# Kernel tuning notes

Hardware: AMD Instinct MI355X
Metric: run time of the kernel (lower is better)

Reference implementation:

```python
import jax, jax.numpy as jnp
import numpy as np

# Module hyperparameters (from init_kwargs)
LATENT = 1024
H = 16          # num query heads
HK = 4          # num key/value heads (GQA)
D = 64          # head_dim
CAUSAL = True
QKV_OUT = (3 * H + 2 * HK) * D  # 3584, as defined in the source module


def setup_inputs() -> dict:
    key = jax.random.key(0)
    k1, k2, k3 = jax.random.split(key, 3)
    B, S = 2, 2048
    x = jax.random.normal(k1, (B, S, LATENT), dtype=jnp.float32)
    # nn.Linear weights are [out_features, in_features]; scale like torch default init
    w_qkv = jax.random.normal(k2, (QKV_OUT, LATENT), dtype=jnp.float32) / np.sqrt(LATENT)
    w_out = jax.random.normal(k3, (LATENT, H * D), dtype=jnp.float32) / np.sqrt(H * D)
    return {"x": x, "w_qkv": w_qkv, "w_out": w_out}


def reference(x, w_qkv, w_out):
    B, S, _ = x.shape
    scale = 1.0 / np.sqrt(D).astype(np.float32)

    # Fused QKV projection: [B,S,(3H+2HK)*D]
    qkv = jnp.einsum('bsl,ol->bso', x, w_qkv)

    # Split: q takes H heads, k and v take HK heads each (GQA).
    # (The extra 2*H*D columns of the fused projection are allocated by the
    #  source module but unused by q/k/v, matching its layer sizing.)
    q = qkv[..., : H * D].reshape(B, S, H, D)
    k = qkv[..., H * D:(H + HK) * D].reshape(B, S, HK, D)
    v = qkv[..., (H + HK) * D:(H + 2 * HK) * D].reshape(B, S, HK, D)

    # Expand KV heads to match query heads (group factor H // HK)
    rep = H // HK
    k = jnp.repeat(k, rep, axis=2)  # [B,S,H,D]
    v = jnp.repeat(v, rep, axis=2)

    # Scaled dot-product attention
    scores = jnp.einsum('bshd,bthd->bhst', q, k) * scale  # [B,H,S,S]
    if CAUSAL:
        causal_mask = jnp.tril(jnp.ones((S, S), dtype=bool))
        scores = jnp.where(causal_mask, scores, jnp.finfo(scores.dtype).min)
    attn = jax.nn.softmax(scores, axis=-1)
    out = jnp.einsum('bhst,bthd->bshd', attn, v).reshape(B, S, H * D)

    # Output projection back to latent_size
    return jnp.einsum('bso,lo->bsl', out, w_out)
```

## Files before the change

kernel.cpp:

```cpp
#include <hip/hip_runtime.h>
#include <hip/hip_bf16.h>
#include <math.h>

typedef __attribute__((ext_vector_type(8))) short bf16x8;
typedef __attribute__((ext_vector_type(4))) float f32x4;
typedef unsigned short u16;
typedef unsigned int   u32;

#define DEVINL __device__ __forceinline__

DEVINL u16 f2bf(float x) {
    u32 u = __float_as_uint(x);
    u += 0x7fffu + ((u >> 16) & 1u);
    return (u16)(u >> 16);
}

DEVINL void gl_lds16(const void* g, void* s) {
    __builtin_amdgcn_global_load_lds(
        (const __attribute__((address_space(1))) u32*)g,
        (__attribute__((address_space(3))) u32*)s,
        16, 0, 0);
}

DEVINL f32x4 mfma16(bf16x8 a, bf16x8 b, f32x4 c) {
    return __builtin_amdgcn_mfma_f32_16x16x32_bf16(a, b, c, 0, 0, 0);
}

__global__ void cvt3(const float* __restrict__ x, const float* __restrict__ wq,
                     const float* __restrict__ wo,
                     u16* __restrict__ xb, u16* __restrict__ wqb, u16* __restrict__ wob) {
    int i = blockIdx.x * 256 + threadIdx.x;
    const float* s; u16* d; int j;
    if (i < 1048576)      { s = x;  d = xb;  j = i; }
    else if (i < 1441792) { s = wq; d = wqb; j = i - 1048576; }
    else                  { s = wo; d = wob; j = i - 1441792; }
    float4 v = ((const float4*)s)[j];
    ushort4 o;
    o.x = f2bf(v.x); o.y = f2bf(v.y); o.z = f2bf(v.z); o.w = f2bf(v.w);
    ((ushort4*)d)[j] = o;
}

template<int EP>
__launch_bounds__(128)
__global__ void gemm_w2(const u16* __restrict__ A, const u16* __restrict__ B,
                        const int N, const int K,
                        float* __restrict__ Cf,
                        u16* __restrict__ Qo, u16* __restrict__ Ko, u16* __restrict__ Vo)
{
    __shared__ __align__(16) u16 As[64 * 64];
    __shared__ __align__(16) u16 Bs[128 * 64];
    const int tid  = threadIdx.x;
    const int lane = tid & 63;
    const int quad = lane >> 4;
    const int lcol = lane & 15;
    const int w    = tid >> 6;
    const int lr   = lane >> 3;
    const int lc   = lane & 7;
    const int swst = lc ^ lr;
    const int rk   = lcol & 7;
    const int m0 = blockIdx.y * 64;
    const int n0 = blockIdx.x * 128;

    f32x4 acc[4][4];
    for (int mb = 0; mb < 4; mb++)
        for (int nb = 0; nb < 4; nb++)
            for (int i = 0; i < 4; i++) acc[mb][nb][i] = 0.f;

    const u16* Ap = A + (m0 + w * 32 + lr) * K + swst * 8;
    const u16* Bp = B + (n0 + w * 64 + lr) * K + swst * 8;

    for (int k0 = 0; k0 < K; k0 += 64) {
        for (int j = 0; j < 4; j++)
            gl_lds16(Ap + j * 8 * K + k0, As + (w * 32 + j * 8) * 64);
        for (int j = 0; j < 8; j++)
            gl_lds16(Bp + j * 8 * K + k0, Bs + (w * 64 + j * 8) * 64);
        __syncthreads();
        bf16x8 af[4][2], bfv[4][2];
        for (int ks = 0; ks < 2; ks++) {
            const int ch = ((ks * 4 + quad) ^ rk) * 8;
            for (int mb = 0; mb < 4; mb++)
                af[mb][ks] = *(const bf16x8*)&As[(mb * 16 + lcol) * 64 + ch];
            for (int nb = 0; nb < 4; nb++)
                bfv[nb][ks] = *(const bf16x8*)&Bs[(w * 64 + nb * 16 + lcol) * 64 + ch];
        }
        for (int ks = 0; ks < 2; ks++)
            for (int mb = 0; mb < 4; mb++)
                for (int nb = 0; nb < 4; nb++)
                    acc[mb][nb] = mfma16(af[mb][ks], bfv[nb][ks], acc[mb][nb]);
        __syncthreads();
    }

    if (EP == 0) {
        for (int mb = 0; mb < 4; mb++)
            for (int nb = 0; nb < 4; nb++) {
                int row = m0 + mb * 16 + quad * 4;
                int col = n0 + w * 64 + nb * 16 + lcol;
                for (int i = 0; i < 4; i++)
                    Cf[(row + i) * N + col] = acc[mb][nb][i];
            }
    } else {
        const float qsc = 0.18033688011112042f;
        for (int mb = 0; mb < 4; mb++)
            for (int nb = 0; nb < 4; nb++)
                for (int i = 0; i < 4; i++) {
                    int row = m0 + mb * 16 + quad * 4 + i;
                    int col = n0 + w * 64 + nb * 16 + lcol;
                    int bb = row >> 11, ss = row & 2047;
                    if (col < 1024) {
                        int hh = col >> 6, dd = col & 63;
                        Qo[((bb * 16 + hh) * 2048 + ss) * 64 + dd] = f2bf(acc[mb][nb][i] * qsc);
                    } else if (col < 1280) {
                        int c = col - 1024, hh = c >> 6, dd = c & 63;
                        Ko[((bb * 4 + hh) * 2048 + ss) * 64 + dd] = f2bf(acc[mb][nb][i]);
                    } else {
                        int c = col - 1280, hh = c >> 6, dd = c & 63;
                        Vo[((bb * 4 + hh) * 64 + dd) * 2048 + ss] = f2bf(acc[mb][nb][i]);
                    }
                }
    }
}

__launch_bounds__(128)
__global__ void attn_kernel(const u16* __restrict__ Qg, const u16* __restrict__ Kg,
                            const u16* __restrict__ Vtg, u16* __restrict__ Og)
{
    __shared__ __align__(16) u16 Ks[2][64 * 64];
    __shared__ __align__(16) u16 Vs[2][64 * 64];
    __shared__ __align__(16) u16 Ps[32 * 64];

    const int tid  = threadIdx.x;
    const int lane = tid & 63;
    const int w    = tid >> 6;
    const int quad = lane >> 4;
    const int lcol = lane & 15;
    const int lr   = lane >> 3;
    const int lc   = lane & 7;
    const int swst = lc ^ lr;
    const int rk   = lcol & 7;

    const int p  = blockIdx.x;
    const int h  = blockIdx.y;
    const int b  = blockIdx.z;
    const int hk = h >> 2;

    const u16* Qp = Qg  + (b * 16 + h) * 2048 * 64;
    const u16* Kp = Kg  + (b * 4 + hk) * 2048 * 64;
    const u16* Vp = Vtg + (b * 4 + hk) * 64 * 2048;

    for (int pass = 0; pass < 2; pass++) {
        const int qi = pass ? (63 - p) : p;
        const int q0 = qi * 32;
        const int nt = (qi >> 1) + 1;

        bf16x8 aqr[2];
        for (int ks = 0; ks < 2; ks++)
            aqr[ks] = *(const bf16x8*)(Qp + (q0 + w * 16 + lcol) * 64 + ks * 32 + quad * 8);

        for (int j = 0; j < 4; j++) {
            const int r = w * 32 + j * 8 + lr;
            gl_lds16(Kp + r * 64 + swst * 8,   &Ks[0][(w * 32 + j * 8) * 64]);
            gl_lds16(Vp + r * 2048 + swst * 8, &Vs[0][(w * 32 + j * 8) * 64]);
        }

        f32x4 o[4];
        float l_p[4];
        for (int db = 0; db < 4; db++)
            for (int i = 0; i < 4; i++) o[db][i] = 0.f;
        for (int i = 0; i < 4; i++) l_p[i] = 0.f;

        __syncthreads();

        for (int ti = 0; ti < nt; ti++) {
            const int cur = ti & 1;
            if (ti + 1 < nt) {
                const int nb = cur ^ 1;
                const int t0n = (ti + 1) * 64;
                for (int j = 0; j < 4; j++) {
                    const int r = w * 32 + j * 8 + lr;
                    gl_lds16(Kp + (t0n + r) * 64 + swst * 8, &Ks[nb][(w * 32 + j * 8) * 64]);
                    gl_lds16(Vp + r * 2048 + t0n + swst * 8, &Vs[nb][(w * 32 + j * 8) * 64]);
                }
            }

            f32x4 s[4];
            for (int cb = 0; cb < 4; cb++)
                for (int i = 0; i < 4; i++) s[cb][i] = 0.f;
            for (int ks = 0; ks < 2; ks++) {
                const int chq = ((ks * 4 + quad) ^ rk) * 8;
                for (int cb = 0; cb < 4; cb++) {
                    bf16x8 bk = *(const bf16x8*)&Ks[cur][(cb * 16 + lcol) * 64 + chq];
                    s[cb] = mfma16(aqr[ks], bk, s[cb]);
                }
            }

            if (ti == nt - 1) {
                const int t0 = ti * 64;
                for (int cb = 0; cb < 4; cb++)
                    for (int i = 0; i < 4; i++) {
                        const int rg = q0 + w * 16 + quad * 4 + i;
                        const int cg = t0 + cb * 16 + lcol;
                        s[cb][i] = (cg > rg) ? -INFINITY : s[cb][i];
                    }
            }

            for (int cb = 0; cb < 4; cb++)
                for (int i = 0; i < 4; i++) {
                    const float pv = exp2f(s[cb][i]);
                    s[cb][i] = pv;
                    l_p[i] += pv;
                }

            for (int cb = 0; cb < 4; cb++)
                for (int i = 0; i < 4; i++) {
                    const int rl = quad * 4 + i;
                    const int cc = cb * 2 + (lcol >> 3);
                    Ps[(w * 16 + rl) * 64 + ((cc ^ (rl & 7)) << 3) + lc] =
                        (u16)(__float_as_uint(s[cb][i]) >> 16);
                }

            for (int kt = 0; kt < 2; kt++) {
                const int chp = ((kt * 4 + quad) ^ rk) * 8;
                bf16x8 ap = *(const bf16x8*)&Ps[(w * 16 + lcol) * 64 + chp];
                for (int db = 0; db < 4; db++) {
                    bf16x8 bv = *(const bf16x8*)&Vs[cur][(db * 16 + lcol) * 64 + chp];
                    o[db] = mfma16(ap, bv, o[db]);
                }
            }
            __syncthreads();
        }

        for (int i = 0; i < 4; i++) {
            float l = l_p[i];
            for (int x = 1; x < 16; x <<= 1) l += __shfl_xor(l, x);
            const float inv = 1.0f / l;
            const int srow = q0 + w * 16 + quad * 4 + i;
            for (int db = 0; db < 4; db++)
                Og[(b * 2048 + srow) * 1024 + h * 64 + db * 16 + lcol] = f2bf(o[db][i] * inv);
        }
    }
}

extern "C" void kernel_launch(void* const* d_in, const int* in_sizes, int n_in,
                              void* d_out, int out_size, void* d_ws, size_t ws_size,
                              hipStream_t stream) {
    const float* x     = (const float*)d_in[0];
    const float* w_qkv = (const float*)d_in[1];
    const float* w_out = (const float*)d_in[2];
    float* out = (float*)d_out;
    char* ws = (char*)d_ws;

    u16* xb  = (u16*)(ws);
    u16* wqb = (u16*)(ws + 8  * 1024 * 1024);
    u16* wob = (u16*)(ws + 11 * 1024 * 1024);
    u16* qb  = (u16*)(ws + 13 * 1024 * 1024);
    u16* kb  = (u16*)(ws + 21 * 1024 * 1024);
    u16* vtb = (u16*)(ws + 23 * 1024 * 1024);
    u16* aob = (u16*)(ws);

    cvt3<<<6656, 256, 0, stream>>>(x, w_qkv, w_out, xb, wqb, wob);

    gemm_w2<1><<<dim3(12, 64), 128, 0, stream>>>(xb, wqb, 1536, 1024,
                                                 nullptr, qb, kb, vtb);
    attn_kernel<<<dim3(32, 16, 2), 128, 0, stream>>>(qb, kb, vtb, aob);
    gemm_w2<0><<<dim3(8, 64), 128, 0, stream>>>(aob, wob, 1024, 1024,
                                                out, nullptr, nullptr, nullptr);
}
```

Measured before the change: 180.9 us.

## Double GEMM K-step to 128 and use 64-row query tiles with 4 waves in attention

The projection GEMM now loads two 64-wide K slices per barrier pair, halving the number of synchronizations per K loop at the cost of doubled LDS. The attention kernel moves from 32-row to 64-row query tiles with 256 threads (4 waves), so each K/V tile loaded into LDS is shared by more query rows and grid size halves. The causal mask is simplified because query and key tiles now align at 64. Fewer blocks and larger LDS may reduce occupancy, and the part of the attention kernel not shown must match the new indexing.

```diff
diff --git a/kernel.cpp b/kernel.cpp
--- a/kernel.cpp
+++ b/kernel.cpp
@@ -47,8 +47,8 @@
                         float* __restrict__ Cf,
                         u16* __restrict__ Qo, u16* __restrict__ Ko, u16* __restrict__ Vo)
 {
-    __shared__ __align__(16) u16 As[64 * 64];
-    __shared__ __align__(16) u16 Bs[128 * 64];
+    __shared__ __align__(16) u16 As[2][64 * 64];
+    __shared__ __align__(16) u16 Bs[2][128 * 64];
     const int tid  = threadIdx.x;
     const int lane = tid & 63;
     const int quad = lane >> 4;
@@ -69,24 +69,27 @@
     const u16* Ap = A + (m0 + w * 32 + lr) * K + swst * 8;
     const u16* Bp = B + (n0 + w * 64 + lr) * K + swst * 8;
 
-    for (int k0 = 0; k0 < K; k0 += 64) {
-        for (int j = 0; j < 4; j++)
-            gl_lds16(Ap + j * 8 * K + k0, As + (w * 32 + j * 8) * 64);
-        for (int j = 0; j < 8; j++)
-            gl_lds16(Bp + j * 8 * K + k0, Bs + (w * 64 + j * 8) * 64);
+    for (int k0 = 0; k0 < K; k0 += 128) {
+        for (int h = 0; h < 2; h++)
+            for (int j = 0; j < 4; j++)
+                gl_lds16(Ap + j * 8 * K + h * 64 + k0, &As[h][(w * 32 + j * 8) * 64]);
+        for (int h = 0; h < 2; h++)
+            for (int j = 0; j < 8; j++)
+                gl_lds16(Bp + j * 8 * K + h * 64 + k0, &Bs[h][(w * 64 + j * 8) * 64]);
         __syncthreads();
-        bf16x8 af[4][2], bfv[4][2];
-        for (int ks = 0; ks < 2; ks++) {
-            const int ch = ((ks * 4 + quad) ^ rk) * 8;
+        for (int ks = 0; ks < 4; ks++) {
+            const int c  = ks * 4 + quad;
+            const int hh = c >> 3;
+            const int ch = ((c & 7) ^ rk) * 8;
+            bf16x8 af[4], bfv[4];
             for (int mb = 0; mb < 4; mb++)
-                af[mb][ks] = *(const bf16x8*)&As[(mb * 16 + lcol) * 64 + ch];
+                af[mb] = *(const bf16x8*)&As[hh][(mb * 16 + lcol) * 64 + ch];
             for (int nb = 0; nb < 4; nb++)
-                bfv[nb][ks] = *(const bf16x8*)&Bs[(w * 64 + nb * 16 + lcol) * 64 + ch];
-        }
-        for (int ks = 0; ks < 2; ks++)
+                bfv[nb] = *(const bf16x8*)&Bs[hh][(w * 64 + nb * 16 + lcol) * 64 + ch];
             for (int mb = 0; mb < 4; mb++)
                 for (int nb = 0; nb < 4; nb++)
-                    acc[mb][nb] = mfma16(af[mb][ks], bfv[nb][ks], acc[mb][nb]);
+                    acc[mb][nb] = mfma16(af[mb], bfv[nb], acc[mb][nb]);
+        }
         __syncthreads();
     }
 
@@ -120,13 +123,13 @@
     }
 }
 
-__launch_bounds__(128)
+__launch_bounds__(256)
 __global__ void attn_kernel(const u16* __restrict__ Qg, const u16* __restrict__ Kg,
                             const u16* __restrict__ Vtg, u16* __restrict__ Og)
 {
     __shared__ __align__(16) u16 Ks[2][64 * 64];
     __shared__ __align__(16) u16 Vs[2][64 * 64];
-    __shared__ __align__(16) u16 Ps[32 * 64];
+    __shared__ __align__(16) u16 Ps[64 * 64];
 
     const int tid  = threadIdx.x;
     const int lane = tid & 63;
@@ -148,18 +151,18 @@
     const u16* Vp = Vtg + (b * 4 + hk) * 64 * 2048;
 
     for (int pass = 0; pass < 2; pass++) {
-        const int qi = pass ? (63 - p) : p;
-        const int q0 = qi * 32;
-        const int nt = (qi >> 1) + 1;
+        const int qi = pass ? (31 - p) : p;
+        const int q0 = qi * 64;
+        const int nt = qi + 1;
 
         bf16x8 aqr[2];
         for (int ks = 0; ks < 2; ks++)
             aqr[ks] = *(const bf16x8*)(Qp + (q0 + w * 16 + lcol) * 64 + ks * 32 + quad * 8);
 
-        for (int j = 0; j < 4; j++) {
-            const int r = w * 32 + j * 8 + lr;
-            gl_lds16(Kp + r * 64 + swst * 8,   &Ks[0][(w * 32 + j * 8) * 64]);
-            gl_lds16(Vp + r * 2048 + swst * 8, &Vs[0][(w * 32 + j * 8) * 64]);
+        for (int j = 0; j < 2; j++) {
+            const int r = w * 16 + j * 8 + lr;
+            gl_lds16(Kp + r * 64 + swst * 8,   &Ks[0][w * 1024 + j * 512]);
+            gl_lds16(Vp + r * 2048 + swst * 8, &Vs[0][w * 1024 + j * 512]);
         }
 
         f32x4 o[4];
@@ -175,10 +178,10 @@
             if (ti + 1 < nt) {
                 const int nb = cur ^ 1;
                 const int t0n = (ti + 1) * 64;
-                for (int j = 0; j < 4; j++) {
-                    const int r = w * 32 + j * 8 + lr;
-                    gl_lds16(Kp + (t0n + r) * 64 + swst * 8, &Ks[nb][(w * 32 + j * 8) * 64]);
-                    gl_lds16(Vp + r * 2048 + t0n + swst * 8, &Vs[nb][(w * 32 + j * 8) * 64]);
+                for (int j = 0; j < 2; j++) {
+                    const int r = w * 16 + j * 8 + lr;
+                    gl_lds16(Kp + (t0n + r) * 64 + swst * 8, &Ks[nb][w * 1024 + j * 512]);
+                    gl_lds16(Vp + r * 2048 + t0n + swst * 8, &Vs[nb][w * 1024 + j * 512]);
                 }
             }
 
@@ -194,12 +197,10 @@
             }
 
             if (ti == nt - 1) {
-                const int t0 = ti * 64;
                 for (int cb = 0; cb < 4; cb++)
                     for (int i = 0; i < 4; i++) {
-                        const int rg = q0 + w * 16 + quad * 4 + i;
-                        const int cg = t0 + cb * 16 + lcol;
-                        s[cb][i] = (cg > rg) ? -INFINITY : s[cb][i];
+                        const bool masked = (cb * 16 + lcol) > (w * 16 + quad * 4 + i);
+                        s[cb][i] = masked ? -INFINITY : s[cb][i];
                     }
             }
 
@@ -261,7 +262,7 @@
 
     gemm_w2<1><<<dim3(12, 64), 128, 0, stream>>>(xb, wqb, 1536, 1024,
                                                  nullptr, qb, kb, vtb);
-    attn_kernel<<<dim3(32, 16, 2), 128, 0, stream>>>(qb, kb, vtb, aob);
+    attn_kernel<<<dim3(16, 16, 2), 256, 0, stream>>>(qb, kb, vtb, aob);
     gemm_w2<0><<<dim3(8, 64), 128, 0, stream>>>(aob, wob, 1024, 1024,
                                                 out, nullptr, nullptr, nullptr);
 }
```

Result: faster. 171.9 us (-5.0%).
